# Performance work log

Hardware: AMD Instinct MI355X
Metric: run time of the kernel (lower is better)

The kernel has to match this reference:

```python
import jax, jax.numpy as jnp
import numpy as np
from jax import lax

RADIUS = (5, 5, 5)
EPS = 1e-5


def _box_sum(x, radius=RADIUS):
    # Separable all-ones box filter == F.conv3d(x, ones((1,1,)+radius), padding='same')
    # x: [N, 1, D, H, W]
    dn = lax.conv_dimension_numbers(x.shape, (1, 1) + radius, ('NCDHW', 'OIDHW', 'NCDHW'))
    for axis, k in zip((2, 3, 4), radius):
        kshape = [1, 1, 1, 1, 1]
        kshape[axis] = k
        kern = jnp.ones(kshape, dtype=x.dtype)
        dn_ax = lax.conv_dimension_numbers(x.shape, tuple(kshape), ('NCDHW', 'OIDHW', 'NCDHW'))
        x = lax.conv_general_dilated(x, kern, window_strides=(1, 1, 1), padding='SAME',
                                     dimension_numbers=dn_ax)
    return x


def _image_gradient(img):
    # torch.gradient over spatial dims (central diff interior, one-sided edges)
    g = jnp.gradient(img, axis=(2, 3, 4))
    return jnp.concatenate(g, axis=1)  # [N, 3, D, H, W]


def setup_inputs() -> dict:
    key = jax.random.key(0)
    k1, k2, k3, k4 = jax.random.split(key, 4)
    shape = (1, 1, 192, 192, 192)
    moving_image = jax.random.normal(k1, shape, dtype=jnp.float32)
    fixed_image = jax.random.normal(k2, shape, dtype=jnp.float32)
    moving_mask = jax.random.randint(k3, shape, 0, 2).astype(jnp.bool_)
    fixed_mask = jax.random.randint(k4, shape, 0, 2).astype(jnp.bool_)
    original_image_spacing = jnp.ones((3,), dtype=jnp.int32)
    return {
        'moving_image': moving_image,
        'fixed_image': fixed_image,
        'moving_mask': moving_mask,
        'fixed_mask': fixed_mask,
        'original_image_spacing': original_image_spacing,
    }


def reference(moving_image, fixed_image, moving_mask, fixed_mask, original_image_spacing):
    npix = float(np.prod(RADIUS))  # 125

    # dual method: union mask applied to both gradients, total grad halved
    union = jnp.logical_or(moving_mask, fixed_mask).astype(moving_image.dtype)
    grad_moving = _image_gradient(moving_image) * union
    grad_fixed = _image_gradient(fixed_image) * union
    total_grad = (grad_moving + grad_fixed) * 0.5

    sum_m = _box_sum(moving_image)
    sum_f = _box_sum(fixed_image)
    sum_mm = _box_sum(moving_image * moving_image)
    sum_ff = _box_sum(fixed_image * fixed_image)
    sum_mf = _box_sum(moving_image * fixed_image)

    moving_mean = sum_m / npix
    fixed_mean = sum_f / npix

    var_m = sum_mm - 2 * moving_mean * sum_m + npix * moving_mean * moving_mean
    var_f = sum_ff - 2 * fixed_mean * sum_f + npix * fixed_mean * fixed_mean
    var_mf = var_m * var_f
    cross = sum_mf - fixed_mean * sum_m - moving_mean * sum_f + npix * moving_mean * fixed_mean

    moving_mean_centered = moving_image - moving_mean
    fixed_mean_centered = fixed_image - fixed_mean

    mask = (var_mf > EPS) & (var_f > EPS) & (fixed_mean_centered != 0.0) & (moving_mean_centered != 0.0)
    var_mf_safe = jnp.where(mask, var_mf, 1.0)
    var_f_safe = jnp.where(mask, var_f, 1.0)
    factor = jnp.where(
        mask,
        2.0 * cross / var_mf_safe * (moving_mean_centered - cross * fixed_mean_centered / var_f_safe),
        0.0,
    )

    return -1.0 * factor * total_grad
```

## Files before the change

kernel.cpp:

```cpp
#include <hip/hip_runtime.h>


#define DD 192
#define HH 192
#define WW 192
#define NVOX (DD * HH * WW)
#define TS 16
#define RR 20
#define RW 24
#define ZSEG 12
#define NBX 12
#define NBY 12
#define NBZ 16
#define PER_XCD ((NBX * NBY * NBZ) / 8)

__global__ __launch_bounds__(256)
void ncc_forces_kernel(const float* __restrict__ mimg,
                       const float* __restrict__ fimg,
                       const int*   __restrict__ mmask,
                       const int*   __restrict__ fmask,
                       float* __restrict__ out)
{
    __shared__ float rawm[5][RR][RW];
    __shared__ float rawf[5][RR][RW];
    __shared__ float xs[5][RR][20];
    __shared__ float box[2][5][TS][20];

    const int b  = blockIdx.x;
    const int L  = (b & 7) * PER_XCD + (b >> 3);
    const int bz = L / (NBX * NBY);
    const int r_ = L - bz * (NBX * NBY);
    const int by = r_ / NBX;
    const int bx = r_ - by * NBX;

    const int tid = threadIdx.x;
    const int tx = tid & 15, ty = tid >> 4;
    const int x0 = bx * TS, y0 = by * TS, z0 = bz * ZSEG;

    const int  simg   = tid / 120;
    const bool stager = (simg < 2);
    const int  st     = tid - simg * 120;
    const int  srow   = st / 6;
    const int  squad  = st - srow * 6;
    const int  sgy    = y0 - 2 + srow;
    const int  sgx    = x0 - 4 + 4 * squad;
    const bool sin_   = (sgy >= 0) && (sgy < HH) && (sgx >= 0) && (sgx <= WW - 4);
    const float* sptr = (simg == 1) ? fimg : mimg;
    float* sldsb = (simg == 1) ? &rawf[0][0][0] : &rawm[0][0][0];
    const int  sloff  = srow * RW + 4 * squad;

    float4 pref = make_float4(0, 0, 0, 0);
    auto prefetch = [&](int zz) {
        pref = make_float4(0, 0, 0, 0);
        if (stager && sin_ && zz >= 0 && zz < DD)
            pref = *(const float4*)(sptr + ((size_t)zz * HH + sgy) * WW + sgx);
    };

    float ring[5][5];
#pragma unroll
    for (int s = 0; s < 5; ++s)
#pragma unroll
        for (int f = 0; f < 5; ++f) ring[s][f] = 0.f;
    float cm[5] = {0, 0, 0, 0, 0}, cf[5] = {0, 0, 0, 0, 0};

    prefetch(z0 - 2);

    for (int n = 0; n <= ZSEG + 4; ++n) {
        const int zc = z0 - 2 + n;
        const int sw = n % 5;
        const int z  = zc - 3;
        const bool emitv = (n >= 5);

        if (stager) *(float4*)(sldsb + sw * (RR * RW) + sloff) = pref;
        prefetch(zc + 1);

        int um = 0, uf = 0;
        int vidx = 0;
        if (emitv) {
            vidx = (z * HH + (y0 + ty)) * WW + (x0 + tx);
            um = __builtin_nontemporal_load(mmask + vidx);
            uf = __builtin_nontemporal_load(fmask + vidx);
        }

        __syncthreads();

        if (tid < 80) {
            const int yy = tid >> 2;
            const int t4 = (tid & 3) * 4;
            const float4 A0 = *(const float4*)&rawm[sw][yy][t4];
            const float4 A1 = *(const float4*)&rawm[sw][yy][t4 + 4];
            const float2 A2 = *(const float2*)&rawm[sw][yy][t4 + 8];
            const float4 B0 = *(const float4*)&rawf[sw][yy][t4];
            const float4 B1 = *(const float4*)&rawf[sw][yy][t4 + 4];
            const float2 B2 = *(const float2*)&rawf[sw][yy][t4 + 8];
            const float a[10] = {A0.x, A0.y, A0.z, A0.w, A1.x, A1.y, A1.z, A1.w, A2.x, A2.y};
            const float bb[10] = {B0.x, B0.y, B0.z, B0.w, B1.x, B1.y, B1.z, B1.w, B2.x, B2.y};
            float p[10], s, w0, w1, w2, w3;
#pragma unroll
            for (int f = 0; f < 5; ++f) {
#pragma unroll
                for (int i = 2; i < 10; ++i) {
                    p[i] = (f == 0) ? a[i] : (f == 1) ? bb[i] :
                           (f == 2) ? a[i] * a[i] : (f == 3) ? bb[i] * bb[i] : a[i] * bb[i];
                }
                s = p[2] + p[3] + p[4] + p[5] + p[6]; w0 = s;
                s += p[7] - p[2]; w1 = s;
                s += p[8] - p[3]; w2 = s;
                s += p[9] - p[4]; w3 = s;
                *(float4*)&xs[f][yy][t4] = make_float4(w0, w1, w2, w3);
            }
        }

        {
            const float ncm = rawm[sw][ty + 2][tx + 4];
            const float ncf = rawf[sw][ty + 2][tx + 4];
#pragma unroll
            for (int s2 = 4; s2 > 0; --s2) { cm[s2] = cm[s2 - 1]; cf[s2] = cf[s2 - 1]; }
            cm[0] = ncm; cf[0] = ncf;
        }
        if (n >= 1) {
            const int pp = (n - 1) & 1;
            float s2d[5];
#pragma unroll
            for (int f = 0; f < 5; ++f) s2d[f] = box[pp][f][tx][ty];
#pragma unroll
            for (int s = 0; s < 4; ++s)
#pragma unroll
                for (int f = 0; f < 5; ++f) ring[s][f] = ring[s + 1][f];
#pragma unroll
            for (int f = 0; f < 5; ++f) ring[4][f] = s2d[f];
        }

        if (emitv) {
            float sum_m = 0.f, sum_f = 0.f, sum_mm = 0.f, sum_ff = 0.f, sum_mf = 0.f;
#pragma unroll
            for (int s = 0; s < 5; ++s) {
                sum_m  += ring[s][0];
                sum_f  += ring[s][1];
                sum_mm += ring[s][2];
                sum_ff += ring[s][3];
                sum_mf += ring[s][4];
            }
            const int gx = x0 + tx, gy = y0 + ty;
            const int s2 = (n + 2) % 5;
            const int cy = ty + 2, cx = tx + 4;
            const float mc = cm[3];
            const float fc = cf[3];

            float gxm, gxf, gym, gyf, gzm, gzf;
            if (gx == 0)          { gxm = rawm[s2][cy][cx + 1] - mc;  gxf = rawf[s2][cy][cx + 1] - fc; }
            else if (gx == WW-1)  { gxm = mc - rawm[s2][cy][cx - 1];  gxf = fc - rawf[s2][cy][cx - 1]; }
            else {
                gxm = 0.5f * (rawm[s2][cy][cx + 1] - rawm[s2][cy][cx - 1]);
                gxf = 0.5f * (rawf[s2][cy][cx + 1] - rawf[s2][cy][cx - 1]);
            }
            if (gy == 0)          { gym = rawm[s2][cy + 1][cx] - mc;  gyf = rawf[s2][cy + 1][cx] - fc; }
            else if (gy == HH-1)  { gym = mc - rawm[s2][cy - 1][cx];  gyf = fc - rawf[s2][cy - 1][cx]; }
            else {
                gym = 0.5f * (rawm[s2][cy + 1][cx] - rawm[s2][cy - 1][cx]);
                gyf = 0.5f * (rawf[s2][cy + 1][cx] - rawf[s2][cy - 1][cx]);
            }
            if (z == 0)           { gzm = cm[2] - mc;             gzf = cf[2] - fc; }
            else if (z == DD-1)   { gzm = mc - cm[4];             gzf = fc - cf[4]; }
            else                  { gzm = 0.5f * (cm[2] - cm[4]); gzf = 0.5f * (cf[2] - cf[4]); }

            const float u = ((um != 0) || (uf != 0)) ? 1.0f : 0.0f;

            const float npix = 125.0f;
            const float inv_npix = 1.0f / 125.0f;
            const float mean_m = sum_m * inv_npix;
            const float mean_f = sum_f * inv_npix;
            const float var_m = sum_mm - 2.0f * mean_m * sum_m + npix * mean_m * mean_m;
            const float var_f = sum_ff - 2.0f * mean_f * sum_f + npix * mean_f * mean_f;
            const float var_mf = var_m * var_f;
            const float cross = sum_mf - mean_f * sum_m - mean_m * sum_f + npix * mean_m * mean_f;
            const float mmc = mc - mean_m;
            const float fmc = fc - mean_f;
            const bool ok = (var_mf > 1e-5f) && (var_f > 1e-5f) && (fmc != 0.0f) && (mmc != 0.0f);
            float factor = 0.0f;
            if (ok) factor = 2.0f * cross / var_mf * (mmc - cross * fmc / var_f);

            const float nf = -factor * 0.5f * u;
            out[vidx]            = nf * (gzm + gzf);
            out[NVOX + vidx]     = nf * (gym + gyf);
            out[2 * NVOX + vidx] = nf * (gxm + gxf);
        }

        __syncthreads();

        if (tid < 160) {
            const int x  = tid & 15;
            const int c8 = ((tid >> 4) & 1) * 8;
            const int f  = tid >> 5;
            float v[12];
#pragma unroll
            for (int j = 0; j < 12; ++j) v[j] = xs[f][c8 + j][x];
            float o[8];
            float s = v[0] + v[1] + v[2] + v[3] + v[4];
            o[0] = s;
#pragma unroll
            for (int j = 1; j < 8; ++j) { s += v[j + 4] - v[j - 1]; o[j] = s; }
            float* bp = &box[n & 1][f][x][c8];
            *(float4*)bp       = make_float4(o[0], o[1], o[2], o[3]);
            *(float4*)(bp + 4) = make_float4(o[4], o[5], o[6], o[7]);
        }
    }
}

extern "C" void kernel_launch(void* const* d_in, const int* in_sizes, int n_in,
                              void* d_out, int out_size, void* d_ws, size_t ws_size,
                              hipStream_t stream)
{
    const float* mimg  = (const float*)d_in[0];
    const float* fimg  = (const float*)d_in[1];
    const int*   mmask = (const int*)d_in[2];
    const int*   fmask = (const int*)d_in[3];
    float* out = (float*)d_out;

    dim3 grid(NBX * NBY * NBZ, 1, 1);
    dim3 block(256, 1, 1);
    hipLaunchKernelGGL(ncc_forces_kernel, grid, block, 0, stream,
                       mimg, fimg, mmask, fmask, out);
}
```

Baseline: 210.2 us.

## Use summed-image gradient slab, longer z segments, and one-step-ahead mask prefetch

Exploits linearity of the gradient by storing a small ring of (moving+fixed) sums and taking one gradient of the summed field instead of two. This shrinks the raw staging buffers from five slices to two. The z segment grows from 12 to 16 slices with fewer blocks, which reduces halo recomputation, and mask loads are issued one iteration ahead to hide latency. It also transposes the box LDS layout to cut bank conflicts and rotates staging thread roles per block to spread wave work. In exchange there is less block-level parallelism (1728 blocks instead of 2304) and different LDS usage.

Measured after the change: 225.6 us. 7.3% more time.

```diff
diff --git a/kernel.cpp b/kernel.cpp
--- a/kernel.cpp
+++ b/kernel.cpp
@@ -5,14 +5,16 @@
 #define HH 192
 #define WW 192
 #define NVOX (DD * HH * WW)
+#define SLICE (HH * WW)
 #define TS 16
 #define RR 20
 #define RW 24
-#define ZSEG 12
+#define ZSEG 16
 #define NBX 12
 #define NBY 12
-#define NBZ 16
-#define PER_XCD ((NBX * NBY * NBZ) / 8)
+#define NBZ 12
+#define NBLK (NBX * NBY * NBZ)
+#define PER_XCD (NBLK / 8)
 
 __global__ __launch_bounds__(256)
 void ncc_forces_kernel(const float* __restrict__ mimg,
@@ -21,10 +23,11 @@
                        const int*   __restrict__ fmask,
                        float* __restrict__ out)
 {
-    __shared__ float rawm[5][RR][RW];
-    __shared__ float rawf[5][RR][RW];
+    __shared__ float rawm[2][RR][RW];
+    __shared__ float rawf[2][RR][RW];
     __shared__ float xs[5][RR][20];
-    __shared__ float box[2][5][TS][20];
+    __shared__ float Tf[4][RR][20];
+    __shared__ float box[2][TS][5][20];
 
     const int b  = blockIdx.x;
     const int L  = (b & 7) * PER_XCD + (b >> 3);
@@ -33,13 +36,14 @@
     const int by = r_ / NBX;
     const int bx = r_ - by * NBX;
 
-    const int tid = threadIdx.x;
+    const int tid  = threadIdx.x;
+    const int rtid = (tid + (((b >> 8) & 3) << 6)) & 255;
     const int tx = tid & 15, ty = tid >> 4;
     const int x0 = bx * TS, y0 = by * TS, z0 = bz * ZSEG;
 
-    const int  simg   = tid / 120;
+    const int  simg   = rtid / 120;
     const bool stager = (simg < 2);
-    const int  st     = tid - simg * 120;
+    const int  st     = rtid - simg * 120;
     const int  srow   = st / 6;
     const int  squad  = st - srow * 6;
     const int  sgy    = y0 - 2 + srow;
@@ -63,37 +67,40 @@
         for (int f = 0; f < 5; ++f) ring[s][f] = 0.f;
     float cm[5] = {0, 0, 0, 0, 0}, cf[5] = {0, 0, 0, 0, 0};
 
+    const int gx = x0 + tx, gy = y0 + ty;
+    const int vbase = (z0 * HH + gy) * WW + gx;
+    int umN = 0, ufN = 0;
+
     prefetch(z0 - 2);
 
     for (int n = 0; n <= ZSEG + 4; ++n) {
         const int zc = z0 - 2 + n;
-        const int sw = n % 5;
+        const int sw = n & 1;
         const int z  = zc - 3;
         const bool emitv = (n >= 5);
 
         if (stager) *(float4*)(sldsb + sw * (RR * RW) + sloff) = pref;
         prefetch(zc + 1);
 
-        int um = 0, uf = 0;
-        int vidx = 0;
-        if (emitv) {
-            vidx = (z * HH + (y0 + ty)) * WW + (x0 + tx);
-            um = __builtin_nontemporal_load(mmask + vidx);
-            uf = __builtin_nontemporal_load(fmask + vidx);
+        const int um = umN, uf = ufN;
+        if (n >= 4 && n < ZSEG + 4) {
+            const int vn = vbase + (n - 4) * SLICE;
+            umN = __builtin_nontemporal_load(mmask + vn);
+            ufN = __builtin_nontemporal_load(fmask + vn);
         }
 
         __syncthreads();
 
-        if (tid < 80) {
-            const int yy = tid >> 2;
-            const int t4 = (tid & 3) * 4;
+        if (rtid < 80) {
+            const int yy = rtid >> 2;
+            const int t4 = (rtid & 3) * 4;
             const float4 A0 = *(const float4*)&rawm[sw][yy][t4];
             const float4 A1 = *(const float4*)&rawm[sw][yy][t4 + 4];
             const float2 A2 = *(const float2*)&rawm[sw][yy][t4 + 8];
             const float4 B0 = *(const float4*)&rawf[sw][yy][t4];
             const float4 B1 = *(const float4*)&rawf[sw][yy][t4 + 4];
             const float2 B2 = *(const float2*)&rawf[sw][yy][t4 + 8];
-            const float a[10] = {A0.x, A0.y, A0.z, A0.w, A1.x, A1.y, A1.z, A1.w, A2.x, A2.y};
+            const float a[10]  = {A0.x, A0.y, A0.z, A0.w, A1.x, A1.y, A1.z, A1.w, A2.x, A2.y};
             const float bb[10] = {B0.x, B0.y, B0.z, B0.w, B1.x, B1.y, B1.z, B1.w, B2.x, B2.y};
             float p[10], s, w0, w1, w2, w3;
 #pragma unroll
@@ -109,6 +116,12 @@
                 s += p[9] - p[4]; w3 = s;
                 *(float4*)&xs[f][yy][t4] = make_float4(w0, w1, w2, w3);
             }
+            const int tw = n & 3;
+            *(float4*)&Tf[tw][yy][t4] =
+                make_float4(a[2] + bb[2], a[3] + bb[3], a[4] + bb[4], a[5] + bb[5]);
+            if (t4 == 12)
+                *(float4*)&Tf[tw][yy][16] =
+                    make_float4(a[6] + bb[6], a[7] + bb[7], a[8] + bb[8], a[9] + bb[9]);
         }
 
         {
@@ -120,15 +133,13 @@
         }
         if (n >= 1) {
             const int pp = (n - 1) & 1;
-            float s2d[5];
-#pragma unroll
-            for (int f = 0; f < 5; ++f) s2d[f] = box[pp][f][tx][ty];
+            const float* bq = &box[pp][tx][0][ty];
+            const float s0 = bq[0], s1 = bq[20], s2v = bq[40], s3 = bq[60], s4 = bq[80];
 #pragma unroll
             for (int s = 0; s < 4; ++s)
 #pragma unroll
                 for (int f = 0; f < 5; ++f) ring[s][f] = ring[s + 1][f];
-#pragma unroll
-            for (int f = 0; f < 5; ++f) ring[4][f] = s2d[f];
+            ring[4][0] = s0; ring[4][1] = s1; ring[4][2] = s2v; ring[4][3] = s3; ring[4][4] = s4;
         }
 
         if (emitv) {
@@ -141,28 +152,29 @@
                 sum_ff += ring[s][3];
                 sum_mf += ring[s][4];
             }
-            const int gx = x0 + tx, gy = y0 + ty;
-            const int s2 = (n + 2) % 5;
-            const int cy = ty + 2, cx = tx + 4;
+            const int vidx = vbase + (n - 5) * SLICE;
+            const int tsl = (n + 1) & 3;
+            const int cy = ty + 2;
             const float mc = cm[3];
             const float fc = cf[3];
-
-            float gxm, gxf, gym, gyf, gzm, gzf;
-            if (gx == 0)          { gxm = rawm[s2][cy][cx + 1] - mc;  gxf = rawf[s2][cy][cx + 1] - fc; }
-            else if (gx == WW-1)  { gxm = mc - rawm[s2][cy][cx - 1];  gxf = fc - rawf[s2][cy][cx - 1]; }
-            else {
-                gxm = 0.5f * (rawm[s2][cy][cx + 1] - rawm[s2][cy][cx - 1]);
-                gxf = 0.5f * (rawf[s2][cy][cx + 1] - rawf[s2][cy][cx - 1]);
-            }
-            if (gy == 0)          { gym = rawm[s2][cy + 1][cx] - mc;  gyf = rawf[s2][cy + 1][cx] - fc; }
-            else if (gy == HH-1)  { gym = mc - rawm[s2][cy - 1][cx];  gyf = fc - rawf[s2][cy - 1][cx]; }
-            else {
-                gym = 0.5f * (rawm[s2][cy + 1][cx] - rawm[s2][cy - 1][cx]);
-                gyf = 0.5f * (rawf[s2][cy + 1][cx] - rawf[s2][cy - 1][cx]);
-            }
-            if (z == 0)           { gzm = cm[2] - mc;             gzf = cf[2] - fc; }
-            else if (z == DD-1)   { gzm = mc - cm[4];             gzf = fc - cf[4]; }
-            else                  { gzm = 0.5f * (cm[2] - cm[4]); gzf = 0.5f * (cf[2] - cf[4]); }
+            const float Tc = mc + fc;
+
+            const float* tp = &Tf[tsl][cy][tx + 1];
+            const float Txm = tp[0], Txp = tp[2];
+            const float* tq = &Tf[tsl][cy - 1][tx + 2];
+            const float Tym = tq[0], Typ = tq[40];
+
+            float gsx, gsy, gsz;
+            if (gx == 0)          gsx = Txp - Tc;
+            else if (gx == WW-1)  gsx = Tc - Txm;
+            else                  gsx = 0.5f * (Txp - Txm);
+            if (gy == 0)          gsy = Typ - Tc;
+            else if (gy == HH-1)  gsy = Tc - Tym;
+            else                  gsy = 0.5f * (Typ - Tym);
+            const float Tzm = cm[4] + cf[4], Tzp = cm[2] + cf[2];
+            if (z == 0)           gsz = Tzp - Tc;
+            else if (z == DD-1)   gsz = Tc - Tzm;
+            else                  gsz = 0.5f * (Tzp - Tzm);
 
             const float u = ((um != 0) || (uf != 0)) ? 1.0f : 0.0f;
 
@@ -181,26 +193,27 @@
             if (ok) factor = 2.0f * cross / var_mf * (mmc - cross * fmc / var_f);
 
             const float nf = -factor * 0.5f * u;
-            out[vidx]            = nf * (gzm + gzf);
-            out[NVOX + vidx]     = nf * (gym + gyf);
-            out[2 * NVOX + vidx] = nf * (gxm + gxf);
+            out[vidx]            = nf * gsz;
+            out[NVOX + vidx]     = nf * gsy;
+            out[2 * NVOX + vidx] = nf * gsx;
         }
 
         __syncthreads();
 
-        if (tid < 160) {
-            const int x  = tid & 15;
-            const int c8 = ((tid >> 4) & 1) * 8;
-            const int f  = tid >> 5;
+        if (rtid < 160) {
+            const int x  = rtid & 15;
+            const int c8 = ((rtid >> 4) & 1) * 8;
+            const int f  = rtid >> 5;
+            const float* xp = &xs[f][c8][x];
             float v[12];
 #pragma unroll
-            for (int j = 0; j < 12; ++j) v[j] = xs[f][c8 + j][x];
+            for (int j = 0; j < 12; ++j) v[j] = xp[20 * j];
             float o[8];
             float s = v[0] + v[1] + v[2] + v[3] + v[4];
             o[0] = s;
 #pragma unroll
             for (int j = 1; j < 8; ++j) { s += v[j + 4] - v[j - 1]; o[j] = s; }
-            float* bp = &box[n & 1][f][x][c8];
+            float* bp = &box[n & 1][x][f][c8];
             *(float4*)bp       = make_float4(o[0], o[1], o[2], o[3]);
             *(float4*)(bp + 4) = make_float4(o[4], o[5], o[6], o[7]);
         }
@@ -217,7 +230,7 @@
     const int*   fmask = (const int*)d_in[3];
     float* out = (float*)d_out;
 
-    dim3 grid(NBX * NBY * NBZ, 1, 1);
+    dim3 grid(NBLK, 1, 1);
     dim3 block(256, 1, 1);
     hipLaunchKernelGGL(ncc_forces_kernel, grid, block, 0, stream,
                        mimg, fimg, mmask, fmask, out);
```
